# Kernel optimization log

Measured on AMD Instinct MI355X. Metric: run time of the kernel, lower is better.

## Reference

```python
import jax, jax.numpy as jnp
import numpy as np

B, C, H, W = 16, 256, 64, 64
NH, AG = 8, 64
KD = C // NH
N = H * W


def _bn_params(k, ch):
    k1, k2, k3, k4 = jax.random.split(k, 4)
    g = 1.0 + 0.1 * jax.random.normal(k1, (ch,), jnp.float32)
    b = 0.1 * jax.random.normal(k2, (ch,), jnp.float32)
    m = 0.1 * jax.random.normal(k3, (ch,), jnp.float32)
    v = jax.random.uniform(k4, (ch,), jnp.float32, 0.5, 1.5)
    return jnp.stack([g, b, m, v])


def setup_inputs() -> dict:
    key = jax.random.key(0)
    ks = jax.random.split(key, 16)
    return {
        "x": jax.random.normal(ks[0], (B, C, H, W), jnp.float32),
        "qkv_w": 0.05 * jax.random.normal(ks[1], (3 * C, C), jnp.float32),
        "qkv_bn": _bn_params(ks[2], 3 * C),
        "pe_w": 0.1 * jax.random.normal(ks[3], (C, 1, 3, 3), jnp.float32),
        "pe_bn": _bn_params(ks[4], C),
        "proj_w": 0.05 * jax.random.normal(ks[5], (C, C), jnp.float32),
        "proj_bn": _bn_params(ks[6], C),
        "an_bias": 0.02 * jax.random.normal(ks[7], (NH, AG, 7, 7), jnp.float32),
        "na_bias": 0.02 * jax.random.normal(ks[8], (NH, AG, 7, 7), jnp.float32),
        "ah_bias": 0.02 * jax.random.normal(ks[9], (1, NH, AG, H, 1), jnp.float32),
        "aw_bias": 0.02 * jax.random.normal(ks[10], (1, NH, AG, 1, W), jnp.float32),
        "ha_bias": 0.02 * jax.random.normal(ks[11], (1, NH, H, 1, AG), jnp.float32),
        "wa_bias": 0.02 * jax.random.normal(ks[12], (1, NH, 1, W, AG), jnp.float32),
    }


def _bn(x, p):
    # inference batchnorm: p = [gamma, beta, running_mean, running_var], eps=1e-5
    g, b, m, v = p
    inv = g * jax.lax.rsqrt(v + 1e-5)
    return (x - m[:, None, None]) * inv[:, None, None] + b[:, None, None]


def reference(x, qkv_w, qkv_bn, pe_w, pe_bn, proj_w, proj_bn,
              an_bias, na_bias, ah_bias, aw_bias, ha_bias, wa_bias):
    scale = KD ** -0.5
    qkv = _bn(jnp.einsum('bchw,oc->bohw', x, qkv_w), qkv_bn)  # [B,3C,H,W]
    qkv = qkv.reshape(B, NH, 3 * KD, N)
    q, k, v = qkv[:, :, :KD], qkv[:, :, KD:2 * KD], qkv[:, :, 2 * KD:]  # [B,NH,KD,N]
    # agent tokens: torch's raw reshape of q to [B,H,W,C], NCHW permute, adaptive avg pool to 8x8
    ps = int(AG ** 0.5)
    ap = q.reshape(B, H, W, C).transpose(0, 3, 1, 2)
    ap = ap.reshape(B, C, ps, H // ps, ps, W // ps).mean(axis=(3, 5)).reshape(B, C, AG)
    a = ap.transpose(0, 2, 1).reshape(B, AG, NH, KD).transpose(0, 2, 3, 1)  # [B,NH,KD,AG]
    # agent -> key attention with interpolated + separable position bias
    pb = (jax.image.resize(an_bias, (NH, AG, H, W), 'bilinear').reshape(1, NH, AG, N)
          + (ah_bias + aw_bias).reshape(1, NH, AG, N))
    attn_k = jax.nn.softmax(jnp.einsum('bhca,bhcn->bhan', a, k) * scale + pb, axis=-1)
    attn = jnp.einsum('bhan,bhcn->bhac', attn_k, v)  # [B,NH,AG,KD]
    # query -> agent attention
    ab = (jax.image.resize(na_bias, (NH, AG, H, W), 'bilinear').reshape(1, NH, AG, N).transpose(0, 1, 3, 2)
          + (ha_bias + wa_bias).reshape(1, NH, N, AG))
    q_attn = jax.nn.softmax(jnp.einsum('bhcn,bhca->bhna', q, a) * scale + ab, axis=-1)
    out = jnp.einsum('bhna,bhac->bhcn', q_attn, attn).reshape(B, C, H, W)
    # depthwise 3x3 positional conv on v + residual
    pe = jax.lax.conv_general_dilated(v.reshape(B, C, H, W), pe_w, (1, 1), 'SAME',
                                      feature_group_count=C,
                                      dimension_numbers=('NCHW', 'OIHW', 'NCHW'))
    out = out + _bn(pe, pe_bn)
    return _bn(jnp.einsum('bchw,oc->bohw', out, proj_w), proj_bn)
```

## Files before the change

kernel.cpp:

```cpp
#include <hip/hip_runtime.h>
#include <cmath>


typedef __bf16 bf16;
typedef bf16 bf16x8 __attribute__((ext_vector_type(8)));
typedef float f32x4 __attribute__((ext_vector_type(4)));

__device__ __forceinline__ f32x4 MFMA16(bf16x8 a, bf16x8 b, f32x4 c) {
  return __builtin_amdgcn_mfma_f32_16x16x32_bf16(a, b, c, 0, 0, 0);
}

__device__ __forceinline__ void gll16(const bf16* g, bf16* l) {
  __builtin_amdgcn_global_load_lds(
      (const __attribute__((address_space(1))) void*)g,
      (__attribute__((address_space(3))) void*)l, 16, 0, 0);
}

constexpr int B_ = 16, C_ = 256, N_ = 4096;
constexpr int NH_ = 8, KD_ = 32, AG_ = 64, O3_ = 768;
constexpr int PSTRIDE_ = 64 + 64 + 64 * 32;
constexpr float SCALE_ = 0.17677669529663687f;

__global__ __launch_bounds__(256) void prep_w_kernel(
    const float* __restrict__ qkv_w, const float* __restrict__ qkv_bn,
    const float* __restrict__ proj_w, const float* __restrict__ proj_bn,
    bf16* __restrict__ wqb, float* __restrict__ shq,
    bf16* __restrict__ wpb, float* __restrict__ shp) {
  int o = blockIdx.x, t = threadIdx.x;
  if (o < O3_) {
    float g = qkv_bn[o], bb = qkv_bn[O3_ + o], m = qkv_bn[2 * O3_ + o],
          v = qkv_bn[3 * O3_ + o];
    float s = g * rsqrtf(v + 1e-5f);
    wqb[(size_t)o * C_ + t] = (bf16)(qkv_w[(size_t)o * C_ + t] * s);
    if (t == 0) shq[o] = bb - m * s;
  } else {
    int p = o - O3_;
    float g = proj_bn[p], bb = proj_bn[C_ + p], m = proj_bn[2 * C_ + p],
          v = proj_bn[3 * C_ + p];
    float s = g * rsqrtf(v + 1e-5f);
    wpb[(size_t)p * C_ + t] = (bf16)(proj_w[(size_t)p * C_ + t] * s);
    if (t == 0) shp[p] = bb - m * s;
  }
}

__device__ __forceinline__ float bilerp7(const float* __restrict__ A, int h, int w) {
  float fy = (h + 0.5f) * (7.0f / 64.0f) - 0.5f;
  float fx = (w + 0.5f) * (7.0f / 64.0f) - 0.5f;
  float fy0 = floorf(fy), fx0 = floorf(fx);
  float wy = fy - fy0, wx = fx - fx0;
  int y0 = (int)fy0, x0 = (int)fx0;
  int y0c = min(max(y0, 0), 6), y1c = min(max(y0 + 1, 0), 6);
  int x0c = min(max(x0, 0), 6), x1c = min(max(x0 + 1, 0), 6);
  float a00 = A[y0c * 7 + x0c], a01 = A[y0c * 7 + x1c];
  float a10 = A[y1c * 7 + x0c], a11 = A[y1c * 7 + x1c];
  return (1.0f - wy) * ((1.0f - wx) * a00 + wx * a01) +
         wy * ((1.0f - wx) * a10 + wx * a11);
}

__global__ __launch_bounds__(256) void bias_pb_kernel(
    const float* __restrict__ an, const float* __restrict__ ah,
    const float* __restrict__ aw, bf16* __restrict__ pb) {
  int tid = blockIdx.x * 256 + threadIdx.x;
  int n = tid & (N_ - 1);
  int g = (tid >> 12) & 63;
  int nh = tid >> 18;
  int h = n >> 6, w = n & 63;
  float v = bilerp7(an + (nh * AG_ + g) * 49, h, w);
  pb[tid] = (bf16)(v + ah[(nh * AG_ + g) * 64 + h] + aw[(nh * AG_ + g) * 64 + w]);
}

__global__ __launch_bounds__(256) void bias_ab_kernel(
    const float* __restrict__ na, const float* __restrict__ ha,
    const float* __restrict__ wa, bf16* __restrict__ ab) {
  int tid = blockIdx.x * 256 + threadIdx.x;
  int g = tid & 63;
  int n = (tid >> 6) & (N_ - 1);
  int nh = tid >> 18;
  int h = n >> 6, w = n & 63;
  float v = bilerp7(na + (nh * AG_ + g) * 49, h, w);
  ab[tid] = (bf16)(v + ha[(nh * 64 + h) * AG_ + g] + wa[(nh * 64 + w) * AG_ + g]);
}

__global__ __launch_bounds__(256) void transpose_x_kernel(
    const float* __restrict__ x, bf16* __restrict__ xT) {
  __shared__ __align__(16) unsigned LDSd[64 * 36];
  int b = blockIdx.x, n0 = blockIdx.y * 64, c0 = blockIdx.z * 64;
  int t = threadIdx.x, n = t & 63, cp = t >> 6;
  const float* xb = x + ((size_t)b * C_ + c0) * N_ + n0;
#pragma unroll
  for (int j = 0; j < 8; j++) {
    int cpr = cp * 8 + j;
    int c = cpr * 2;
    float f0 = xb[(size_t)c * N_ + n];
    float f1 = xb[(size_t)(c + 1) * N_ + n];
    union { bf16 h[2]; unsigned u; } pk;
    pk.h[0] = (bf16)f0; pk.h[1] = (bf16)f1;
    LDSd[n * 36 + cpr] = pk.u;
  }
  __syncthreads();
  int n2 = t >> 2, seg = t & 3;
  const unsigned* row = &LDSd[n2 * 36 + seg * 8];
  uint4 d0 = *(const uint4*)row;
  uint4 d1 = *(const uint4*)(row + 4);
  bf16* dst = xT + ((size_t)b * N_ + n0 + n2) * C_ + c0 + seg * 16;
  *(uint4*)dst = d0;
  *(uint4*)(dst + 8) = d1;
}

__global__ __launch_bounds__(256) void qkv_gemm_kernel(
    const bf16* __restrict__ xT, const bf16* __restrict__ wqb,
    const float* __restrict__ shq, bf16* __restrict__ qT,
    bf16* __restrict__ kT, bf16* __restrict__ vv) {
  int nt = blockIdx.x * 128, ot = blockIdx.y * 128, b = blockIdx.z;
  __shared__ __align__(16) bf16 As[128][32];
  __shared__ __align__(16) bf16 Bs[128][32];
  int t = threadIdx.x, wave = t >> 6, lane = t & 63, quad = lane >> 4, l16 = lane & 15;
  int wm = (wave >> 1) * 64, wn = (wave & 1) * 64;
  int lr = lane >> 2, lc = (lane & 3) * 8;
  f32x4 acc[4][4];
#pragma unroll
  for (int mi = 0; mi < 4; mi++)
#pragma unroll
    for (int ni = 0; ni < 4; ni++) acc[mi][ni] = (f32x4){0.f, 0.f, 0.f, 0.f};
  const bf16* xTb = xT + (size_t)b * N_ * C_;
  for (int k0 = 0; k0 < 256; k0 += 32) {
    __syncthreads();
#pragma unroll
    for (int i = 0; i < 2; i++) {
      int r0 = wave * 32 + i * 16;
      gll16(wqb + (size_t)(ot + r0 + lr) * C_ + k0 + lc, &As[r0][0]);
      gll16(xTb + (size_t)(nt + r0 + lr) * C_ + k0 + lc, &Bs[r0][0]);
    }
    __syncthreads();
    bf16x8 af[4], bfv[4];
#pragma unroll
    for (int mi = 0; mi < 4; mi++)
      af[mi] = *(const bf16x8*)&As[wm + mi * 16 + l16][quad * 8];
#pragma unroll
    for (int ni = 0; ni < 4; ni++)
      bfv[ni] = *(const bf16x8*)&Bs[wn + ni * 16 + l16][quad * 8];
#pragma unroll
    for (int mi = 0; mi < 4; mi++)
#pragma unroll
      for (int ni = 0; ni < 4; ni++)
        acc[mi][ni] = MFMA16(af[mi], bfv[ni], acc[mi][ni]);
  }
#pragma unroll
  for (int mi = 0; mi < 4; mi++) {
    int o0 = ot + wm + mi * 16 + quad * 4;
    float4 s4 = *(const float4*)(shq + o0);
    float sh[4] = {s4.x, s4.y, s4.z, s4.w};
    int base16 = ot + wm + mi * 16;
    int nh = base16 / 96;
    int rem = base16 % 96;
    int type = rem >> 5;
    int kdb = (rem & 31) + quad * 4;
    if (type < 2) {
      bf16* dst = (type == 0 ? qT : kT) + ((size_t)(b * NH_ + nh) * N_) * KD_;
#pragma unroll
      for (int ni = 0; ni < 4; ni++) {
        int n = nt + wn + ni * 16 + l16;
        union { ushort4 u; bf16 e[4]; } pk;
#pragma unroll
        for (int r = 0; r < 4; r++) pk.e[r] = (bf16)(acc[mi][ni][r] + sh[r]);
        *(ushort4*)(dst + (size_t)n * KD_ + kdb) = pk.u;
      }
    } else {
      bf16* dst = vv + ((size_t)(b * NH_ + nh) * KD_) * N_;
#pragma unroll
      for (int ni = 0; ni < 4; ni++) {
        int n = nt + wn + ni * 16 + l16;
#pragma unroll
        for (int r = 0; r < 4; r++)
          dst[(size_t)(kdb + r) * N_ + n] = (bf16)(acc[mi][ni][r] + sh[r]);
      }
    }
  }
}

__global__ __launch_bounds__(256) void pool_kernel(
    const bf16* __restrict__ qT, bf16* __restrict__ aT) {
  int tid = blockIdx.x * 256 + threadIdx.x;
  int kd2 = tid & 31;
  int g = (tid >> 5) & 63;
  int nh2 = (tid >> 11) & 7;
  int b = tid >> 14;
  int c = nh2 * KD_ + kd2;
  int ho = g >> 3, wo = g & 7;
  int ww = c & 63, ch = c >> 6;
  const bf16* qb = qT + ((size_t)(b * NH_ + ho) * N_) * KD_;
  float s = 0.f;
#pragma unroll
  for (int wi = 0; wi < 8; wi++) {
    int w_ = wo * 8 + wi;
    int n1 = ((w_ & 15) * 4 + ch) * 64 + ww;
    int kdlo = w_ >> 4;
#pragma unroll
    for (int hi = 0; hi < 8; hi++)
      s += (float)qb[(size_t)n1 * KD_ + kdlo + hi * 4];
  }
  aT[tid] = (bf16)(s * (1.0f / 64.0f));
}

struct SM3comb { float m[4][64]; float l[4][64]; float o[4][64][32]; };
union SM3u { bf16 Ps[4][64][72]; SM3comb c; };

__global__ __launch_bounds__(256) void attn1_kernel(
    const bf16* __restrict__ kT, const bf16* __restrict__ vv,
    const bf16* __restrict__ aT, const bf16* __restrict__ pb,
    float* __restrict__ part) {
  __shared__ __align__(16) SM3u sm;
  int tile = blockIdx.x, bh = blockIdx.y, nh = bh & 7;
  int t = threadIdx.x, wave = t >> 6, lane = t & 63, quad = lane >> 4, l16 = lane & 15;
  const bf16* aTb = aT + (size_t)bh * (AG_ * KD_);
  const bf16* kb = kT + (size_t)bh * N_ * KD_;
  const bf16* vb = vv + (size_t)bh * KD_ * N_;
  const bf16* pbh = pb + (size_t)nh * AG_ * N_;
  int nloc = wave * 64, ng = tile * 256 + nloc;
  bf16x8 af[4], kf[4];
#pragma unroll
  for (int mi = 0; mi < 4; mi++)
    af[mi] = *(const bf16x8*)(aTb + (mi * 16 + l16) * KD_ + quad * 8);
#pragma unroll
  for (int ni = 0; ni < 4; ni++)
    kf[ni] = *(const bf16x8*)(kb + (size_t)(ng + ni * 16 + l16) * KD_ + quad * 8);
  float mrow[4][4], lrow[4][4];
  f32x4 zero4 = (f32x4){0.f, 0.f, 0.f, 0.f};
#pragma unroll
  for (int mi = 0; mi < 4; mi++) {
    f32x4 s[4];
#pragma unroll
    for (int ni = 0; ni < 4; ni++) s[ni] = MFMA16(af[mi], kf[ni], zero4);
    int g0 = mi * 16 + quad * 4;
#pragma unroll
    for (int ni = 0; ni < 4; ni++) {
      const bf16* p = pbh + (size_t)g0 * N_ + ng + ni * 16 + l16;
#pragma unroll
      for (int r = 0; r < 4; r++)
        s[ni][r] = s[ni][r] * SCALE_ + (float)p[(size_t)r * N_];
    }
#pragma unroll
    for (int r = 0; r < 4; r++) {
      float mx = fmaxf(fmaxf(s[0][r], s[1][r]), fmaxf(s[2][r], s[3][r]));
#pragma unroll
      for (int off = 1; off < 16; off <<= 1) mx = fmaxf(mx, __shfl_xor(mx, off));
      float rs = 0.f;
#pragma unroll
      for (int ni = 0; ni < 4; ni++) {
        float pv = __expf(s[ni][r] - mx);
        s[ni][r] = pv; rs += pv;
      }
#pragma unroll
      for (int off = 1; off < 16; off <<= 1) rs += __shfl_xor(rs, off);
      mrow[mi][r] = mx; lrow[mi][r] = rs;
    }
#pragma unroll
    for (int ni = 0; ni < 4; ni++)
#pragma unroll
      for (int r = 0; r < 4; r++)
        sm.Ps[wave][mi * 16 + quad * 4 + r][ni * 16 + l16] = (bf16)s[ni][r];
  }
  f32x4 oacc[4][2];
#pragma unroll
  for (int mi = 0; mi < 4; mi++) { oacc[mi][0] = zero4; oacc[mi][1] = zero4; }
#pragma unroll
  for (int ks = 0; ks < 2; ks++) {
    bf16x8 vf[2], pf[4];
#pragma unroll
    for (int ci = 0; ci < 2; ci++)
      vf[ci] = *(const bf16x8*)(vb + (size_t)(ci * 16 + l16) * N_ + ng + ks * 32 + quad * 8);
#pragma unroll
    for (int mi = 0; mi < 4; mi++)
      pf[mi] = *(const bf16x8*)&sm.Ps[wave][mi * 16 + l16][ks * 32 + quad * 8];
#pragma unroll
    for (int mi = 0; mi < 4; mi++)
#pragma unroll
      for (int ci = 0; ci < 2; ci++)
        oacc[mi][ci] = MFMA16(pf[mi], vf[ci], oacc[mi][ci]);
  }
  __syncthreads();
#pragma unroll
  for (int mi = 0; mi < 4; mi++)
#pragma unroll
    for (int r = 0; r < 4; r++) {
      int g = mi * 16 + quad * 4 + r;
      if (l16 == 0) { sm.c.m[wave][g] = mrow[mi][r]; sm.c.l[wave][g] = lrow[mi][r]; }
      sm.c.o[wave][g][l16] = oacc[mi][0][r];
      sm.c.o[wave][g][16 + l16] = oacc[mi][1][r];
    }
  __syncthreads();
  {
    int g = t >> 2, kd0 = (t & 3) * 8;
    float M = fmaxf(fmaxf(sm.c.m[0][g], sm.c.m[1][g]), fmaxf(sm.c.m[2][g], sm.c.m[3][g]));
    float ew[4], L = 0.f;
#pragma unroll
    for (int w2 = 0; w2 < 4; w2++) {
      ew[w2] = __expf(sm.c.m[w2][g] - M);
      L += sm.c.l[w2][g] * ew[w2];
    }
    float* pt = part + (size_t)(bh * 16 + tile) * PSTRIDE_;
    if ((t & 3) == 0) { pt[g] = M; pt[64 + g] = L; }
    float4 o0, o1;
    o0.x = o0.y = o0.z = o0.w = 0.f; o1 = o0;
#pragma unroll
    for (int w2 = 0; w2 < 4; w2++) {
      float e = ew[w2];
      const float* src = &sm.c.o[w2][g][kd0];
      o0.x += src[0] * e; o0.y += src[1] * e; o0.z += src[2] * e; o0.w += src[3] * e;
      o1.x += src[4] * e; o1.y += src[5] * e; o1.z += src[6] * e; o1.w += src[7] * e;
    }
    *(float4*)(pt + 128 + g * 32 + kd0) = o0;
    *(float4*)(pt + 128 + g * 32 + kd0 + 4) = o1;
  }
}

__global__ __launch_bounds__(256) void attn1_combine_kernel(
    const float* __restrict__ part, bf16* __restrict__ attnT) {
  int bh = blockIdx.x, t = threadIdx.x;
  int g = t >> 2, kd0 = (t & 3) * 8;
  const float* base = part + (size_t)bh * 16 * PSTRIDE_;
  float gm = -1e30f, L = 0.f;
  float o[8];
#pragma unroll
  for (int j = 0; j < 8; j++) o[j] = 0.f;
  for (int tl = 0; tl < 16; tl++) {
    const float* pt = base + tl * PSTRIDE_;
    float m = pt[g], l = pt[64 + g];
    float nm = fmaxf(gm, m);
    float a0 = __expf(gm - nm), a1 = __expf(m - nm);
    L = L * a0 + l * a1;
    float4 x0 = *(const float4*)(pt + 128 + g * 32 + kd0);
    float4 x1 = *(const float4*)(pt + 128 + g * 32 + kd0 + 4);
    o[0] = o[0] * a0 + x0.x * a1; o[1] = o[1] * a0 + x0.y * a1;
    o[2] = o[2] * a0 + x0.z * a1; o[3] = o[3] * a0 + x0.w * a1;
    o[4] = o[4] * a0 + x1.x * a1; o[5] = o[5] * a0 + x1.y * a1;
    o[6] = o[6] * a0 + x1.z * a1; o[7] = o[7] * a0 + x1.w * a1;
    gm = nm;
  }
  float inv = 1.0f / L;
  bf16* dst = attnT + (size_t)bh * (KD_ * AG_);
#pragma unroll
  for (int j = 0; j < 8; j++)
    dst[(kd0 + j) * AG_ + g] = (bf16)(o[j] * inv);
}

__global__ __launch_bounds__(256) void attn2_kernel(
    const bf16* __restrict__ qT, const bf16* __restrict__ aT,
    const bf16* __restrict__ attnT, const bf16* __restrict__ ab,
    bf16* __restrict__ outa) {
  __shared__ __align__(16) bf16 Ps[4][64][72];
  int nt = blockIdx.x * 256;
  int bh = blockIdx.y, b = bh >> 3, nh = bh & 7;
  int t = threadIdx.x, wave = t >> 6, lane = t & 63, quad = lane >> 4, l16 = lane & 15;
  const bf16* qb = qT + (size_t)bh * N_ * KD_;
  const bf16* aTb = aT + (size_t)bh * (AG_ * KD_);
  const bf16* atb = attnT + (size_t)bh * (KD_ * AG_);
  bf16x8 afr[4], tfr[2][2];
#pragma unroll
  for (int gi = 0; gi < 4; gi++)
    afr[gi] = *(const bf16x8*)(aTb + (gi * 16 + l16) * KD_ + quad * 8);
#pragma unroll
  for (int ci = 0; ci < 2; ci++)
#pragma unroll
    for (int ks = 0; ks < 2; ks++)
      tfr[ci][ks] = *(const bf16x8*)(atb + (ci * 16 + l16) * AG_ + ks * 32 + quad * 8);
  const bf16* abh = ab + (size_t)nh * N_ * AG_;
  int nloc = wave * 64;
  f32x4 zero4 = (f32x4){0.f, 0.f, 0.f, 0.f};
#pragma unroll
  for (int mi = 0; mi < 4; mi++) {
    bf16x8 qf = *(const bf16x8*)(qb + (size_t)(nt + nloc + mi * 16 + l16) * KD_ + quad * 8);
    f32x4 s[4];
#pragma unroll
    for (int gi = 0; gi < 4; gi++)
      s[gi] = MFMA16(qf, afr[gi], zero4);
    int n0 = nt + nloc + mi * 16 + quad * 4;
#pragma unroll
    for (int gi = 0; gi < 4; gi++) {
      int g = gi * 16 + l16;
#pragma unroll
      for (int r = 0; r < 4; r++)
        s[gi][r] = s[gi][r] * SCALE_ + (float)abh[(size_t)(n0 + r) * AG_ + g];
    }
#pragma unroll
    for (int r = 0; r < 4; r++) {
      float mx = fmaxf(fmaxf(s[0][r], s[1][r]), fmaxf(s[2][r], s[3][r]));
#pragma unroll
      for (int off = 1; off < 16; off <<= 1) mx = fmaxf(mx, __shfl_xor(mx, off));
      float rs = 0.f;
#pragma unroll
      for (int gi = 0; gi < 4; gi++) {
        float p = __expf(s[gi][r] - mx);
        s[gi][r] = p; rs += p;
      }
#pragma unroll
      for (int off = 1; off < 16; off <<= 1) rs += __shfl_xor(rs, off);
      float inv = 1.0f / rs;
#pragma unroll
      for (int gi = 0; gi < 4; gi++) s[gi][r] *= inv;
    }
#pragma unroll
    for (int gi = 0; gi < 4; gi++)
#pragma unroll
      for (int r = 0; r < 4; r++)
        Ps[wave][mi * 16 + quad * 4 + r][gi * 16 + l16] = (bf16)s[gi][r];
  }
  __syncthreads();
  f32x4 O[4][2];
#pragma unroll
  for (int mi = 0; mi < 4; mi++) { O[mi][0] = zero4; O[mi][1] = zero4; }
#pragma unroll
  for (int ks = 0; ks < 2; ks++) {
    bf16x8 pf[4];
#pragma unroll
    for (int mi = 0; mi < 4; mi++)
      pf[mi] = *(const bf16x8*)&Ps[wave][mi * 16 + l16][ks * 32 + quad * 8];
#pragma unroll
    for (int mi = 0; mi < 4; mi++)
#pragma unroll
      for (int ci = 0; ci < 2; ci++)
        O[mi][ci] = MFMA16(pf[mi], tfr[ci][ks], O[mi][ci]);
  }
  bf16* ob = outa + (size_t)b * C_ * N_;
#pragma unroll
  for (int mi = 0; mi < 4; mi++) {
    int n0 = nt + nloc + mi * 16 + quad * 4;
#pragma unroll
    for (int ci = 0; ci < 2; ci++) {
      int c = nh * KD_ + ci * 16 + l16;
      union { ushort4 u; bf16 e[4]; } pk;
#pragma unroll
      for (int r = 0; r < 4; r++) pk.e[r] = (bf16)O[mi][ci][r];
      *(ushort4*)(ob + (size_t)c * N_ + n0) = pk.u;
    }
  }
}

__global__ __launch_bounds__(256) void pe_tr_kernel(
    const bf16* __restrict__ vv, const bf16* __restrict__ outa,
    const float* __restrict__ pw, const float* __restrict__ bn,
    bf16* __restrict__ hT) {
  __shared__ __align__(16) bf16 Vs[3][64][68];
  __shared__ __align__(16) bf16 Os[64][68];
  int b = blockIdx.x, n0 = blockIdx.y * 64, c0 = blockIdx.z * 64;
  int h = n0 >> 6;
  int t = threadIdx.x;
#pragma unroll
  for (int dy = 0; dy < 3; dy++) {
    int hh = h + dy - 1;
    bool ok = (unsigned)hh < 64u;
#pragma unroll
    for (int it = 0; it < 2; it++) {
      int u = it * 256 + t;
      int c = u >> 3, seg = u & 7;
      union { uint4 q; uint2 d[2]; } val;
      val.q = make_uint4(0u, 0u, 0u, 0u);
      if (ok)
        val.q = *(const uint4*)(vv + ((size_t)b * C_ + c0 + c) * N_ + hh * 64 + seg * 8);
      *(uint2*)&Vs[dy][c][seg * 8] = val.d[0];
      *(uint2*)&Vs[dy][c][seg * 8 + 4] = val.d[1];
    }
  }
#pragma unroll
  for (int it = 0; it < 2; it++) {
    int u = it * 256 + t;
    int c = u >> 3, seg = u & 7;
    union { uint4 q; uint2 d[2]; } val;
    val.q = *(const uint4*)(outa + ((size_t)b * C_ + c0 + c) * N_ + n0 + seg * 8);
    *(uint2*)&Os[c][seg * 8] = val.d[0];
    *(uint2*)&Os[c][seg * 8 + 4] = val.d[1];
  }
  __syncthreads();
  int cl = t & 63, wv = t >> 6;
  int c = c0 + cl;
  const float* wc = pw + c * 9;
  float w00 = wc[0], w01 = wc[1], w02 = wc[2];
  float w10 = wc[3], w11 = wc[4], w12 = wc[5];
  float w20 = wc[6], w21 = wc[7], w22 = wc[8];
  float sc = bn[c] * rsqrtf(bn[3 * C_ + c] + 1e-5f);
  float sh = bn[C_ + c] - bn[2 * C_ + c] * sc;
#pragma unroll
  for (int half = 0; half < 2; half++) {
    int oct = half * 4 + wv;
    int w0 = oct * 8;
    float r[3][10];
#pragma unroll
    for (int dy = 0; dy < 3; dy++) {
      union { uint2 q; bf16 e[4]; } lo, hi;
      lo.q = *(const uint2*)&Vs[dy][cl][w0];
      hi.q = *(const uint2*)&Vs[dy][cl][w0 + 4];
#pragma unroll
      for (int j = 0; j < 4; j++) {
        r[dy][j + 1] = (float)lo.e[j];
        r[dy][j + 5] = (float)hi.e[j];
      }
      r[dy][0] = (w0 > 0) ? (float)Vs[dy][cl][w0 - 1] : 0.f;
      r[dy][9] = (w0 < 56) ? (float)Vs[dy][cl][w0 + 8] : 0.f;
    }
    union { uint2 q; bf16 e[4]; } plo, phi;
    plo.q = *(const uint2*)&Os[cl][w0];
    phi.q = *(const uint2*)&Os[cl][w0 + 4];
    bf16* dst = hT + ((size_t)b * N_ + n0 + w0) * C_ + c;
#pragma unroll
    for (int j = 0; j < 8; j++) {
      float a = r[0][j] * w00 + r[0][j + 1] * w01 + r[0][j + 2] * w02 +
                r[1][j] * w10 + r[1][j + 1] * w11 + r[1][j + 2] * w12 +
                r[2][j] * w20 + r[2][j + 1] * w21 + r[2][j + 2] * w22;
      float po = (j < 4) ? (float)plo.e[j] : (float)phi.e[j - 4];
      dst[(size_t)j * C_] = (bf16)(po + a * sc + sh);
    }
  }
}

__global__ __launch_bounds__(256) void proj_gemm_kernel(
    const bf16* __restrict__ hT, const bf16* __restrict__ wpb,
    const float* __restrict__ shp, float* __restrict__ out) {
  int nt = blockIdx.x * 128, ot = blockIdx.y * 128, b = blockIdx.z;
  __shared__ __align__(16) bf16 As[128][32];
  __shared__ __align__(16) bf16 Bs[128][32];
  int t = threadIdx.x, wave = t >> 6, lane = t & 63, quad = lane >> 4, l16 = lane & 15;
  int wm = (wave >> 1) * 64, wn = (wave & 1) * 64;
  int lr = lane >> 2, lc = (lane & 3) * 8;
  f32x4 acc[4][4];
#pragma unroll
  for (int mi = 0; mi < 4; mi++)
#pragma unroll
    for (int ni = 0; ni < 4; ni++) acc[mi][ni] = (f32x4){0.f, 0.f, 0.f, 0.f};
  const bf16* hTb = hT + (size_t)b * N_ * C_;
  for (int k0 = 0; k0 < 256; k0 += 32) {
    __syncthreads();
#pragma unroll
    for (int i = 0; i < 2; i++) {
      int r0 = wave * 32 + i * 16;
      gll16(wpb + (size_t)(ot + r0 + lr) * C_ + k0 + lc, &As[r0][0]);
      gll16(hTb + (size_t)(nt + r0 + lr) * C_ + k0 + lc, &Bs[r0][0]);
    }
    __syncthreads();
    bf16x8 af[4], bfv[4];
#pragma unroll
    for (int mi = 0; mi < 4; mi++)
      af[mi] = *(const bf16x8*)&As[wm + mi * 16 + l16][quad * 8];
#pragma unroll
    for (int ni = 0; ni < 4; ni++)
      bfv[ni] = *(const bf16x8*)&Bs[wn + ni * 16 + l16][quad * 8];
#pragma unroll
    for (int mi = 0; mi < 4; mi++)
#pragma unroll
      for (int ni = 0; ni < 4; ni++)
        acc[mi][ni] = MFMA16(af[mi], bfv[ni], acc[mi][ni]);
  }
  float* ob = out + (size_t)b * C_ * N_;
#pragma unroll
  for (int mi = 0; mi < 4; mi++) {
    int o0 = ot + wm + mi * 16 + quad * 4;
    float4 s4 = *(const float4*)(shp + o0);
    float sh[4] = {s4.x, s4.y, s4.z, s4.w};
#pragma unroll
    for (int ni = 0; ni < 4; ni++) {
      int n = nt + wn + ni * 16 + l16;
#pragma unroll
      for (int r = 0; r < 4; r++)
        ob[(size_t)(o0 + r) * N_ + n] = acc[mi][ni][r] + sh[r];
    }
  }
}

extern "C" void kernel_launch(void* const* d_in, const int* in_sizes, int n_in,
                              void* d_out, int out_size, void* d_ws, size_t ws_size,
                              hipStream_t stream) {
  const float* x = (const float*)d_in[0];
  const float* qkv_w = (const float*)d_in[1];
  const float* qkv_bn = (const float*)d_in[2];
  const float* pe_w = (const float*)d_in[3];
  const float* pe_bn = (const float*)d_in[4];
  const float* proj_w = (const float*)d_in[5];
  const float* proj_bn = (const float*)d_in[6];
  const float* an_bias = (const float*)d_in[7];
  const float* na_bias = (const float*)d_in[8];
  const float* ah_bias = (const float*)d_in[9];
  const float* aw_bias = (const float*)d_in[10];
  const float* ha_bias = (const float*)d_in[11];
  const float* wa_bias = (const float*)d_in[12];

  char* ws = (char*)d_ws;
  bf16* qT = (bf16*)(ws + 0);
  bf16* kT = (bf16*)(ws + 33554432);
  bf16* vv = (bf16*)(ws + 67108864);
  bf16* pb = (bf16*)(ws + 100663296);
  bf16* ab = (bf16*)(ws + 104857600);
  bf16* aT = (bf16*)(ws + 109051904);
  bf16* attnT = (bf16*)(ws + 109576192);
  bf16* outa = (bf16*)(ws + 110100480);
  bf16* wqb = (bf16*)(ws + 143654912);
  bf16* wpb = (bf16*)(ws + 144048128);
  float* shq = (float*)(ws + 144179200);
  float* shp = (float*)(ws + 144183296);
  bf16* xT = outa;
  bf16* houT = kT;
  float* part = (float*)outa;

  prep_w_kernel<<<1024, 256, 0, stream>>>(qkv_w, qkv_bn, proj_w, proj_bn,
                                          wqb, shq, wpb, shp);
  bias_pb_kernel<<<8192, 256, 0, stream>>>(an_bias, ah_bias, aw_bias, pb);
  bias_ab_kernel<<<8192, 256, 0, stream>>>(na_bias, ha_bias, wa_bias, ab);
  transpose_x_kernel<<<dim3(16, 64, 4), 256, 0, stream>>>(x, xT);
  qkv_gemm_kernel<<<dim3(32, 6, 16), 256, 0, stream>>>(xT, wqb, shq, qT, kT, vv);
  pool_kernel<<<1024, 256, 0, stream>>>(qT, aT);
  attn1_kernel<<<dim3(16, 128), 256, 0, stream>>>(kT, vv, aT, pb, part);
  attn1_combine_kernel<<<128, 256, 0, stream>>>(part, attnT);
  attn2_kernel<<<dim3(16, 128), 256, 0, stream>>>(qT, aT, attnT, ab, outa);
  pe_tr_kernel<<<dim3(16, 64, 4), 256, 0, stream>>>(vv, outa, pe_w, pe_bn, houT);
  proj_gemm_kernel<<<dim3(32, 2, 16), 256, 0, stream>>>(houT, wpb, shp,
                                                        (float*)d_out);
}
```

Measured before the change: 367.8 us.

## Double-buffer LDS tiles and XOR-swizzle columns in QKV and proj GEMMs

Both 1x1-conv GEMM kernels now keep two LDS buffers, so the global-to-LDS load of the next K slice is issued before the MFMAs on the current slice, and one barrier per step replaces two. The 16-byte column chunks are also XOR-swizzled by row on both the load and the read side, to cut LDS bank conflicts on the fragment reads. This doubles LDS use per block, which may lower occupancy. It also relies on the global_load_lds writes being complete at the barrier, since there is no explicit vmcnt wait.

```diff
diff --git a/kernel.cpp b/kernel.cpp
--- a/kernel.cpp
+++ b/kernel.cpp
@@ -112,38 +112,53 @@
     const float* __restrict__ shq, bf16* __restrict__ qT,
     bf16* __restrict__ kT, bf16* __restrict__ vv) {
   int nt = blockIdx.x * 128, ot = blockIdx.y * 128, b = blockIdx.z;
-  __shared__ __align__(16) bf16 As[128][32];
-  __shared__ __align__(16) bf16 Bs[128][32];
+  __shared__ __align__(16) bf16 As[2][128][32];
+  __shared__ __align__(16) bf16 Bs[2][128][32];
   int t = threadIdx.x, wave = t >> 6, lane = t & 63, quad = lane >> 4, l16 = lane & 15;
   int wm = (wave >> 1) * 64, wn = (wave & 1) * 64;
-  int lr = lane >> 2, lc = (lane & 3) * 8;
+  int lr = lane >> 2;
+  int lsw = ((lane & 3) ^ ((lr >> 1) & 3)) * 8;
+  int rsw = (l16 >> 1) & 3;
   f32x4 acc[4][4];
 #pragma unroll
   for (int mi = 0; mi < 4; mi++)
 #pragma unroll
     for (int ni = 0; ni < 4; ni++) acc[mi][ni] = (f32x4){0.f, 0.f, 0.f, 0.f};
   const bf16* xTb = xT + (size_t)b * N_ * C_;
-  for (int k0 = 0; k0 < 256; k0 += 32) {
-    __syncthreads();
-#pragma unroll
-    for (int i = 0; i < 2; i++) {
-      int r0 = wave * 32 + i * 16;
-      gll16(wqb + (size_t)(ot + r0 + lr) * C_ + k0 + lc, &As[r0][0]);
-      gll16(xTb + (size_t)(nt + r0 + lr) * C_ + k0 + lc, &Bs[r0][0]);
-    }
-    __syncthreads();
+#pragma unroll
+  for (int i = 0; i < 2; i++) {
+    int r0 = wave * 32 + i * 16;
+    gll16(wqb + (size_t)(ot + r0 + lr) * C_ + lsw, &As[0][r0][0]);
+    gll16(xTb + (size_t)(nt + r0 + lr) * C_ + lsw, &Bs[0][r0][0]);
+  }
+  __syncthreads();
+  int cur = 0;
+  for (int ks = 0; ks < 8; ks++) {
+    if (ks < 7) {
+      int k0 = (ks + 1) * 32;
+#pragma unroll
+      for (int i = 0; i < 2; i++) {
+        int r0 = wave * 32 + i * 16;
+        gll16(wqb + (size_t)(ot + r0 + lr) * C_ + k0 + lsw, &As[cur ^ 1][r0][0]);
+        gll16(xTb + (size_t)(nt + r0 + lr) * C_ + k0 + lsw, &Bs[cur ^ 1][r0][0]);
+      }
+    }
     bf16x8 af[4], bfv[4];
 #pragma unroll
     for (int mi = 0; mi < 4; mi++)
-      af[mi] = *(const bf16x8*)&As[wm + mi * 16 + l16][quad * 8];
+      af[mi] = *(const bf16x8*)&As[cur][wm + mi * 16 + l16][(quad ^ rsw) * 8];
 #pragma unroll
     for (int ni = 0; ni < 4; ni++)
-      bfv[ni] = *(const bf16x8*)&Bs[wn + ni * 16 + l16][quad * 8];
+      bfv[ni] = *(const bf16x8*)&Bs[cur][wn + ni * 16 + l16][(quad ^ rsw) * 8];
 #pragma unroll
     for (int mi = 0; mi < 4; mi++)
 #pragma unroll
       for (int ni = 0; ni < 4; ni++)
         acc[mi][ni] = MFMA16(af[mi], bfv[ni], acc[mi][ni]);
+    if (ks < 7) {
+      __syncthreads();
+      cur ^= 1;
+    }
   }
 #pragma unroll
   for (int mi = 0; mi < 4; mi++) {
@@ -516,38 +531,53 @@
     const bf16* __restrict__ hT, const bf16* __restrict__ wpb,
     const float* __restrict__ shp, float* __restrict__ out) {
   int nt = blockIdx.x * 128, ot = blockIdx.y * 128, b = blockIdx.z;
-  __shared__ __align__(16) bf16 As[128][32];
-  __shared__ __align__(16) bf16 Bs[128][32];
+  __shared__ __align__(16) bf16 As[2][128][32];
+  __shared__ __align__(16) bf16 Bs[2][128][32];
   int t = threadIdx.x, wave = t >> 6, lane = t & 63, quad = lane >> 4, l16 = lane & 15;
   int wm = (wave >> 1) * 64, wn = (wave & 1) * 64;
-  int lr = lane >> 2, lc = (lane & 3) * 8;
+  int lr = lane >> 2;
+  int lsw = ((lane & 3) ^ ((lr >> 1) & 3)) * 8;
+  int rsw = (l16 >> 1) & 3;
   f32x4 acc[4][4];
 #pragma unroll
   for (int mi = 0; mi < 4; mi++)
 #pragma unroll
     for (int ni = 0; ni < 4; ni++) acc[mi][ni] = (f32x4){0.f, 0.f, 0.f, 0.f};
   const bf16* hTb = hT + (size_t)b * N_ * C_;
-  for (int k0 = 0; k0 < 256; k0 += 32) {
-    __syncthreads();
-#pragma unroll
-    for (int i = 0; i < 2; i++) {
-      int r0 = wave * 32 + i * 16;
-      gll16(wpb + (size_t)(ot + r0 + lr) * C_ + k0 + lc, &As[r0][0]);
-      gll16(hTb + (size_t)(nt + r0 + lr) * C_ + k0 + lc, &Bs[r0][0]);
-    }
-    __syncthreads();
+#pragma unroll
+  for (int i = 0; i < 2; i++) {
+    int r0 = wave * 32 + i * 16;
+    gll16(wpb + (size_t)(ot + r0 + lr) * C_ + lsw, &As[0][r0][0]);
+    gll16(hTb + (size_t)(nt + r0 + lr) * C_ + lsw, &Bs[0][r0][0]);
+  }
+  __syncthreads();
+  int cur = 0;
+  for (int ks = 0; ks < 8; ks++) {
+    if (ks < 7) {
+      int k0 = (ks + 1) * 32;
+#pragma unroll
+      for (int i = 0; i < 2; i++) {
+        int r0 = wave * 32 + i * 16;
+        gll16(wpb + (size_t)(ot + r0 + lr) * C_ + k0 + lsw, &As[cur ^ 1][r0][0]);
+        gll16(hTb + (size_t)(nt + r0 + lr) * C_ + k0 + lsw, &Bs[cur ^ 1][r0][0]);
+      }
+    }
     bf16x8 af[4], bfv[4];
 #pragma unroll
     for (int mi = 0; mi < 4; mi++)
-      af[mi] = *(const bf16x8*)&As[wm + mi * 16 + l16][quad * 8];
+      af[mi] = *(const bf16x8*)&As[cur][wm + mi * 16 + l16][(quad ^ rsw) * 8];
 #pragma unroll
     for (int ni = 0; ni < 4; ni++)
-      bfv[ni] = *(const bf16x8*)&Bs[wn + ni * 16 + l16][quad * 8];
+      bfv[ni] = *(const bf16x8*)&Bs[cur][wn + ni * 16 + l16][(quad ^ rsw) * 8];
 #pragma unroll
     for (int mi = 0; mi < 4; mi++)
 #pragma unroll
       for (int ni = 0; ni < 4; ni++)
         acc[mi][ni] = MFMA16(af[mi], bfv[ni], acc[mi][ni]);
+    if (ks < 7) {
+      __syncthreads();
+      cur ^= 1;
+    }
   }
   float* ob = out + (size_t)b * C_ * N_;
 #pragma unroll
```

Result: no change. 368.6 us (+0.2%).
